# Optimization experiments

Measured on AMD Instinct MI355X. Metric: run time of the kernel, lower is better.

The kernel has to match this reference:

```python
import jax, jax.numpy as jnp
import numpy as np

NUM_CAPSULE = 16
DIM_CAPSULE = 64
ROUTINGS = 3
T_EPS = 1e-7


def setup_inputs() -> dict:
    key = jax.random.key(0)
    k1, k2 = jax.random.split(key)
    x = jax.random.normal(k1, (64, 512, 768), dtype=jnp.float32)
    # xavier-normal-ish init for W: [1, input_dim_capsule, num_capsule*dim_capsule]
    fan_in, fan_out = 768, NUM_CAPSULE * DIM_CAPSULE
    std = float(np.sqrt(2.0 / (fan_in + fan_out)))
    W = jax.random.normal(k2, (1, 768, NUM_CAPSULE * DIM_CAPSULE), dtype=jnp.float32) * std
    return {"x": x, "W": W}


def _squash(v, eps=T_EPS):
    # NOTE: this module's 'squash' is pure L2 normalization with eps, not the
    # classic (s^2/(1+s^2)) squash.
    s2 = jnp.sum(v * v, axis=-1, keepdims=True)
    return v / jnp.sqrt(s2 + eps)


def reference(x, W):
    B, In, _ = x.shape
    # u_hat: [B, In, num*dim] -> [B, num, In, dim]
    u = jnp.matmul(x, W).reshape(B, In, NUM_CAPSULE, DIM_CAPSULE).transpose(0, 2, 1, 3)
    b = jnp.zeros((B, NUM_CAPSULE, In), dtype=u.dtype)  # routing logits
    outputs = None
    for i in range(ROUTINGS):
        # torch code softmaxes over the num_capsule axis (after permute dance)
        c = jax.nn.softmax(b, axis=1)  # [B, num, In]
        outputs = _squash(jnp.einsum('bij,bijk->bik', c, u))  # [B, num, dim]
        if i < ROUTINGS - 1:
            b = jnp.einsum('bik,bijk->bij', outputs, u)  # [B, num, In]
    return outputs
```

## Files before the change

### kernel.cpp

```cpp
#include <hip/hip_runtime.h>
#include <hip/hip_bf16.h>
#include <stdint.h>

#define BATCH 64
#define IN_CAPS 512
#define NCAP 16
#define DCAP 64
#define GN (NCAP * DCAP)
#define GM (BATCH * IN_CAPS)
#define GK 768

typedef __bf16 bf16;
typedef __attribute__((ext_vector_type(8))) __bf16 bf16x8;
typedef __attribute__((ext_vector_type(4))) __bf16 bf16x4;
typedef __attribute__((ext_vector_type(4))) float f32x4;

__global__ void k_detect(const uint32_t* __restrict__ X32, int* __restrict__ flag) {
    const int lane = threadIdx.x;
    int cnt = 0;
#pragma unroll
    for (int i = 0; i < 4; ++i) {
        const uint32_t w = X32[lane * 4 + i];
        const uint32_t e = (w >> 7) & 0xFF;
        cnt += (e >= 119 && e <= 130) ? 1 : 0;
    }
#pragma unroll
    for (int off = 32; off >= 1; off >>= 1) cnt += __shfl_xor(cnt, off);
    if (lane == 0) *flag = (cnt > 128) ? 1 : 0;
}

template <typename T>
__global__ void k_transW(const T* __restrict__ W, bf16* __restrict__ Wt,
                         const int* __restrict__ flag, int want) {
    if (*flag != want) return;
    __shared__ bf16 t[32][33];
    const int k0 = blockIdx.x * 32;
    const int n0 = blockIdx.y * 32;
    const int tx = threadIdx.x, ty = threadIdx.y;
#pragma unroll
    for (int r = 0; r < 4; ++r)
        t[ty + r * 8][tx] = (bf16)(float)W[(size_t)(k0 + ty + r * 8) * GN + n0 + tx];
    __syncthreads();
#pragma unroll
    for (int r = 0; r < 4; ++r)
        Wt[(size_t)(n0 + ty + r * 8) * GK + k0 + tx] = t[tx][ty + r * 8];
}

__device__ inline bf16x8 load8(const bf16* p) { return *(const bf16x8*)p; }
__device__ inline bf16x8 load8(const float* p) {
    const f32x4 a = *(const f32x4*)p;
    const f32x4 b = *(const f32x4*)(p + 4);
    bf16x8 r;
    r[0] = (bf16)a[0]; r[1] = (bf16)a[1]; r[2] = (bf16)a[2]; r[3] = (bf16)a[3];
    r[4] = (bf16)b[0]; r[5] = (bf16)b[1]; r[6] = (bf16)b[2]; r[7] = (bf16)b[3];
    return r;
}

template <typename T>
__global__ __launch_bounds__(256) void k_gemm(const T* __restrict__ X,
                                              const bf16* __restrict__ Wt,
                                              bf16* __restrict__ U,
                                              const int* __restrict__ flag, int want) {
    if (*flag != want) return;
    __shared__ bf16 sA[128 * 32];
    __shared__ bf16 sB[128 * 32];

    const int tid = threadIdx.x;
    const int lane = tid & 63;
    const int wave = tid >> 6;
    const int wm = wave >> 1, wn = wave & 1;
    const int m0 = blockIdx.x * 128;
    const int n0 = blockIdx.y * 128;

    const int srow = tid >> 2;
    const int scol = (tid & 3) * 8;

    f32x4 acc[4][4] = {};

    const int fr = lane & 15;
    const int fq = lane >> 4;

    for (int kt = 0; kt < GK / 32; ++kt) {
        const int kb = kt * 32;
        const bf16x8 a0 = load8(X + (size_t)(m0 + srow) * GK + kb + scol);
        const bf16x8 a1 = load8(X + (size_t)(m0 + srow + 64) * GK + kb + scol);
        const bf16x8 b0 = load8(Wt + (size_t)(n0 + srow) * GK + kb + scol);
        const bf16x8 b1 = load8(Wt + (size_t)(n0 + srow + 64) * GK + kb + scol);

        __syncthreads();
        *(bf16x8*)(sA + srow * 32 + scol) = a0;
        *(bf16x8*)(sA + (srow + 64) * 32 + scol) = a1;
        *(bf16x8*)(sB + srow * 32 + scol) = b0;
        *(bf16x8*)(sB + (srow + 64) * 32 + scol) = b1;
        __syncthreads();

        bf16x8 af[4], bfr[4];
#pragma unroll
        for (int mi = 0; mi < 4; ++mi)
            af[mi] = *(const bf16x8*)(sA + (wm * 64 + mi * 16 + fr) * 32 + fq * 8);
#pragma unroll
        for (int ni = 0; ni < 4; ++ni)
            bfr[ni] = *(const bf16x8*)(sB + (wn * 64 + ni * 16 + fr) * 32 + fq * 8);
#pragma unroll
        for (int mi = 0; mi < 4; ++mi)
#pragma unroll
            for (int ni = 0; ni < 4; ++ni)
                acc[mi][ni] = __builtin_amdgcn_mfma_f32_16x16x32_bf16(
                    af[mi], bfr[ni], acc[mi][ni], 0, 0, 0);
    }

#pragma unroll
    for (int mi = 0; mi < 4; ++mi) {
#pragma unroll
        for (int ni = 0; ni < 4; ++ni) {
#pragma unroll
            for (int r = 0; r < 4; ++r) {
                const int m = m0 + wm * 64 + mi * 16 + fq * 4 + r;
                const int n = n0 + wn * 64 + ni * 16 + fr;
                const int bb = m >> 9, j = m & 511;
                const int ci = n >> 6, k = n & 63;
                U[(((size_t)(bb * NCAP + ci)) * IN_CAPS + j) * DCAP + k] =
                    (bf16)acc[mi][ni][r];
            }
        }
    }
}

__global__ __launch_bounds__(256) void k_caps_out(const bf16* __restrict__ U,
                                                  const float* __restrict__ C,
                                                  float* __restrict__ OutF,
                                                  float* __restrict__ OutC,
                                                  int useC) {
    const int bi = blockIdx.x;
    const int tid = threadIdx.x;
    const int lane = tid & 63, wave = tid >> 6;
    const int kq = lane & 15, jj = lane >> 4;
    const size_t ubase = (size_t)bi * IN_CAPS * DCAP;

    float a0 = 0.f, a1 = 0.f, a2 = 0.f, a3 = 0.f;
#pragma unroll 4
    for (int it = 0; it < 32; ++it) {
        const int j = it * 16 + wave * 4 + jj;
        const bf16x4 v = *(const bf16x4*)(U + ubase + (size_t)j * DCAP + kq * 4);
        const float cv = useC ? C[(size_t)bi * IN_CAPS + j] : 0.0625f;
        a0 += cv * (float)v[0];
        a1 += cv * (float)v[1];
        a2 += cv * (float)v[2];
        a3 += cv * (float)v[3];
    }

    __shared__ float red[16][64];
    const int p = wave * 4 + jj;
    red[p][kq * 4 + 0] = a0;
    red[p][kq * 4 + 1] = a1;
    red[p][kq * 4 + 2] = a2;
    red[p][kq * 4 + 3] = a3;
    __syncthreads();

    if (wave == 0) {
        float s = 0.f;
#pragma unroll
        for (int q = 0; q < 16; ++q) s += red[q][lane];
        float ss = s * s;
#pragma unroll
        for (int off = 32; off >= 1; off >>= 1) ss += __shfl_xor(ss, off);
        const float val = s * rsqrtf(ss + 1e-7f);
        OutF[(size_t)bi * DCAP + lane] = val;
        OutC[(size_t)bi * DCAP + lane] = val;
    }
}

__global__ __launch_bounds__(256) void k_caps_logits(const bf16* __restrict__ U,
                                                     const float* __restrict__ OutF,
                                                     float* __restrict__ BL) {
    const int bi = blockIdx.x;
    const int tid = threadIdx.x;
    const int lane = tid & 63, wave = tid >> 6;
    const int kq = lane & 15, jj = lane >> 4;
    const size_t ubase = (size_t)bi * IN_CAPS * DCAP;

    const float4 ov = *(const float4*)(OutF + (size_t)bi * DCAP + kq * 4);
#pragma unroll 4
    for (int it = 0; it < 32; ++it) {
        const int j = it * 16 + wave * 4 + jj;
        const bf16x4 v = *(const bf16x4*)(U + ubase + (size_t)j * DCAP + kq * 4);
        float p = ov.x * (float)v[0] + ov.y * (float)v[1] +
                  ov.z * (float)v[2] + ov.w * (float)v[3];
        p += __shfl_xor(p, 1);
        p += __shfl_xor(p, 2);
        p += __shfl_xor(p, 4);
        p += __shfl_xor(p, 8);
        if (kq == 0) BL[(size_t)bi * IN_CAPS + j] = p;
    }
}

__global__ __launch_bounds__(256) void k_softmax(float* __restrict__ BL) {
    const int t = blockIdx.x * 256 + threadIdx.x;
    const int b = t >> 9, j = t & 511;
    float* p = BL + (size_t)b * NCAP * IN_CAPS + j;
    float v[16];
    float m = -1e30f;
#pragma unroll
    for (int i = 0; i < 16; ++i) {
        v[i] = p[(size_t)i * IN_CAPS];
        m = fmaxf(m, v[i]);
    }
    float s = 0.f;
#pragma unroll
    for (int i = 0; i < 16; ++i) {
        v[i] = __expf(v[i] - m);
        s += v[i];
    }
    const float inv = 1.0f / s;
#pragma unroll
    for (int i = 0; i < 16; ++i) p[(size_t)i * IN_CAPS] = v[i] * inv;
}

extern "C" void kernel_launch(void* const* d_in, const int* in_sizes, int n_in,
                              void* d_out, int out_size, void* d_ws, size_t ws_size,
                              hipStream_t stream) {
    float* OutC = (float*)d_out;

    const size_t u_bytes = (size_t)BATCH * NCAP * IN_CAPS * DCAP * sizeof(bf16);
    const size_t wt_bytes = (size_t)GN * GK * sizeof(bf16);
    const size_t outf_bytes = (size_t)BATCH * NCAP * DCAP * sizeof(float);
    const size_t bl_bytes = (size_t)BATCH * NCAP * IN_CAPS * sizeof(float);
    char* ws = (char*)d_ws;
    bf16* U = (bf16*)ws;
    bf16* Wt = (bf16*)(ws + u_bytes);
    float* OutF = (float*)(ws + u_bytes + wt_bytes);
    float* BL = (float*)(ws + u_bytes + wt_bytes + outf_bytes);
    int* flag = (int*)(ws + u_bytes + wt_bytes + outf_bytes + bl_bytes);
    if (ws_size < u_bytes + wt_bytes + outf_bytes + bl_bytes + 256) return;

    k_detect<<<1, 64, 0, stream>>>((const uint32_t*)d_in[0], flag);

    k_transW<bf16><<<dim3(GK / 32, GN / 32), dim3(32, 8), 0, stream>>>(
        (const bf16*)d_in[1], Wt, flag, 1);
    k_transW<float><<<dim3(GK / 32, GN / 32), dim3(32, 8), 0, stream>>>(
        (const float*)d_in[1], Wt, flag, 0);

    k_gemm<bf16><<<dim3(GM / 128, GN / 128), 256, 0, stream>>>(
        (const bf16*)d_in[0], Wt, U, flag, 1);
    k_gemm<float><<<dim3(GM / 128, GN / 128), 256, 0, stream>>>(
        (const float*)d_in[0], Wt, U, flag, 0);

    k_caps_out<<<BATCH * NCAP, 256, 0, stream>>>(U, BL, OutF, OutC, 0);
    k_caps_logits<<<BATCH * NCAP, 256, 0, stream>>>(U, OutF, BL);
    k_softmax<<<BATCH * IN_CAPS / 256, 256, 0, stream>>>(BL);
    k_caps_out<<<BATCH * NCAP, 256, 0, stream>>>(U, BL, OutF, OutC, 1);
    k_caps_logits<<<BATCH * NCAP, 256, 0, stream>>>(U, OutF, BL);
    k_softmax<<<BATCH * IN_CAPS / 256, 256, 0, stream>>>(BL);
    k_caps_out<<<BATCH * NCAP, 256, 0, stream>>>(U, BL, OutF, OutC, 1);
}
```

Measured before the change: 298.0 us.

## Pre-convert X to bf16, use async global-to-LDS GEMM loads, fuse routing kernels

Adds a separate pass that converts X to bf16 in workspace, so the GEMM can use direct global-to-LDS loads (global_load_lds) instead of register staging. It also fuses the caps_out and caps_logits kernels into one routing kernel that caches each capsule's 64KB U slice in LDS, so U is read once per iteration instead of twice. The costs are an extra full read and write of X for the conversion, more workspace, and heavy LDS use that limits occupancy in the routing kernel. A fallback keeps the old inline GEMM path when workspace is small.

```diff
diff --git a/kernel.cpp b/kernel.cpp
--- a/kernel.cpp
+++ b/kernel.cpp
@@ -15,6 +15,12 @@
 typedef __attribute__((ext_vector_type(4))) __bf16 bf16x4;
 typedef __attribute__((ext_vector_type(4))) float f32x4;
 
+__device__ inline void async16(const bf16* g, bf16* l) {
+    __builtin_amdgcn_global_load_lds(
+        (__attribute__((address_space(1))) void*)g,
+        (__attribute__((address_space(3))) void*)l, 16, 0, 0);
+}
+
 __global__ void k_detect(const uint32_t* __restrict__ X32, int* __restrict__ flag) {
     const int lane = threadIdx.x;
     int cnt = 0;
@@ -27,6 +33,25 @@
 #pragma unroll
     for (int off = 32; off >= 1; off >>= 1) cnt += __shfl_xor(cnt, off);
     if (lane == 0) *flag = (cnt > 128) ? 1 : 0;
+}
+
+__device__ inline bf16x8 load8(const bf16* p) { return *(const bf16x8*)p; }
+__device__ inline bf16x8 load8(const float* p) {
+    const f32x4 a = *(const f32x4*)p;
+    const f32x4 b = *(const f32x4*)(p + 4);
+    bf16x8 r;
+    r[0] = (bf16)a[0]; r[1] = (bf16)a[1]; r[2] = (bf16)a[2]; r[3] = (bf16)a[3];
+    r[4] = (bf16)b[0]; r[5] = (bf16)b[1]; r[6] = (bf16)b[2]; r[7] = (bf16)b[3];
+    return r;
+}
+
+template <typename T>
+__global__ __launch_bounds__(256) void k_convX(const T* __restrict__ X,
+                                               bf16* __restrict__ Xb,
+                                               const int* __restrict__ flag, int want) {
+    if (*flag != want) return;
+    const size_t i = ((size_t)blockIdx.x * 256 + threadIdx.x) * 8;
+    *(bf16x8*)(Xb + i) = load8(X + i);
 }
 
 template <typename T>
@@ -46,22 +71,9 @@
         Wt[(size_t)(n0 + ty + r * 8) * GK + k0 + tx] = t[tx][ty + r * 8];
 }
 
-__device__ inline bf16x8 load8(const bf16* p) { return *(const bf16x8*)p; }
-__device__ inline bf16x8 load8(const float* p) {
-    const f32x4 a = *(const f32x4*)p;
-    const f32x4 b = *(const f32x4*)(p + 4);
-    bf16x8 r;
-    r[0] = (bf16)a[0]; r[1] = (bf16)a[1]; r[2] = (bf16)a[2]; r[3] = (bf16)a[3];
-    r[4] = (bf16)b[0]; r[5] = (bf16)b[1]; r[6] = (bf16)b[2]; r[7] = (bf16)b[3];
-    return r;
-}
-
-template <typename T>
-__global__ __launch_bounds__(256) void k_gemm(const T* __restrict__ X,
-                                              const bf16* __restrict__ Wt,
-                                              bf16* __restrict__ U,
-                                              const int* __restrict__ flag, int want) {
-    if (*flag != want) return;
+__global__ __launch_bounds__(256) void k_gemm_async(const bf16* __restrict__ Xb,
+                                                    const bf16* __restrict__ Wt,
+                                                    bf16* __restrict__ U) {
     __shared__ bf16 sA[128 * 32];
     __shared__ bf16 sB[128 * 32];
 
@@ -72,26 +84,28 @@
     const int m0 = blockIdx.x * 128;
     const int n0 = blockIdx.y * 128;
 
-    const int srow = tid >> 2;
-    const int scol = (tid & 3) * 8;
+    const int c0 = wave * 2, c1 = wave * 2 + 1;
+    const int rl = lane >> 2, cl = (lane & 3) * 8;
+    const bf16* gA0 = Xb + (size_t)(m0 + c0 * 16 + rl) * GK + cl;
+    const bf16* gA1 = Xb + (size_t)(m0 + c1 * 16 + rl) * GK + cl;
+    const bf16* gB0 = Wt + (size_t)(n0 + c0 * 16 + rl) * GK + cl;
+    const bf16* gB1 = Wt + (size_t)(n0 + c1 * 16 + rl) * GK + cl;
+    bf16* lA0 = sA + c0 * 512;
+    bf16* lA1 = sA + c1 * 512;
+    bf16* lB0 = sB + c0 * 512;
+    bf16* lB1 = sB + c1 * 512;
 
     f32x4 acc[4][4] = {};
-
     const int fr = lane & 15;
     const int fq = lane >> 4;
 
     for (int kt = 0; kt < GK / 32; ++kt) {
-        const int kb = kt * 32;
-        const bf16x8 a0 = load8(X + (size_t)(m0 + srow) * GK + kb + scol);
-        const bf16x8 a1 = load8(X + (size_t)(m0 + srow + 64) * GK + kb + scol);
-        const bf16x8 b0 = load8(Wt + (size_t)(n0 + srow) * GK + kb + scol);
-        const bf16x8 b1 = load8(Wt + (size_t)(n0 + srow + 64) * GK + kb + scol);
-
         __syncthreads();
-        *(bf16x8*)(sA + srow * 32 + scol) = a0;
-        *(bf16x8*)(sA + (srow + 64) * 32 + scol) = a1;
-        *(bf16x8*)(sB + srow * 32 + scol) = b0;
-        *(bf16x8*)(sB + (srow + 64) * 32 + scol) = b1;
+        async16(gA0, lA0);
+        async16(gA1, lA1);
+        async16(gB0, lB0);
+        async16(gB1, lB1);
+        gA0 += 32; gA1 += 32; gB0 += 32; gB1 += 32;
         __syncthreads();
 
         bf16x8 af[4], bfr[4];
@@ -126,30 +140,110 @@
     }
 }
 
-__global__ __launch_bounds__(256) void k_caps_out(const bf16* __restrict__ U,
-                                                  const float* __restrict__ C,
-                                                  float* __restrict__ OutF,
-                                                  float* __restrict__ OutC,
-                                                  int useC) {
+template <typename T>
+__global__ __launch_bounds__(256) void k_gemm_inline(const T* __restrict__ X,
+                                                     const bf16* __restrict__ Wt,
+                                                     bf16* __restrict__ U,
+                                                     const int* __restrict__ flag,
+                                                     int want) {
+    if (*flag != want) return;
+    __shared__ bf16 sA[128 * 32];
+    __shared__ bf16 sB[128 * 32];
+    const int tid = threadIdx.x;
+    const int lane = tid & 63;
+    const int wave = tid >> 6;
+    const int wm = wave >> 1, wn = wave & 1;
+    const int m0 = blockIdx.x * 128;
+    const int n0 = blockIdx.y * 128;
+    const int srow = tid >> 2;
+    const int scol = (tid & 3) * 8;
+    f32x4 acc[4][4] = {};
+    const int fr = lane & 15;
+    const int fq = lane >> 4;
+    for (int kt = 0; kt < GK / 32; ++kt) {
+        const int kb = kt * 32;
+        const bf16x8 a0 = load8(X + (size_t)(m0 + srow) * GK + kb + scol);
+        const bf16x8 a1 = load8(X + (size_t)(m0 + srow + 64) * GK + kb + scol);
+        const bf16x8 b0 = load8(Wt + (size_t)(n0 + srow) * GK + kb + scol);
+        const bf16x8 b1 = load8(Wt + (size_t)(n0 + srow + 64) * GK + kb + scol);
+        __syncthreads();
+        *(bf16x8*)(sA + srow * 32 + scol) = a0;
+        *(bf16x8*)(sA + (srow + 64) * 32 + scol) = a1;
+        *(bf16x8*)(sB + srow * 32 + scol) = b0;
+        *(bf16x8*)(sB + (srow + 64) * 32 + scol) = b1;
+        __syncthreads();
+        bf16x8 af[4], bfr[4];
+#pragma unroll
+        for (int mi = 0; mi < 4; ++mi)
+            af[mi] = *(const bf16x8*)(sA + (wm * 64 + mi * 16 + fr) * 32 + fq * 8);
+#pragma unroll
+        for (int ni = 0; ni < 4; ++ni)
+            bfr[ni] = *(const bf16x8*)(sB + (wn * 64 + ni * 16 + fr) * 32 + fq * 8);
+#pragma unroll
+        for (int mi = 0; mi < 4; ++mi)
+#pragma unroll
+            for (int ni = 0; ni < 4; ++ni)
+                acc[mi][ni] = __builtin_amdgcn_mfma_f32_16x16x32_bf16(
+                    af[mi], bfr[ni], acc[mi][ni], 0, 0, 0);
+    }
+#pragma unroll
+    for (int mi = 0; mi < 4; ++mi) {
+#pragma unroll
+        for (int ni = 0; ni < 4; ++ni) {
+#pragma unroll
+            for (int r = 0; r < 4; ++r) {
+                const int m = m0 + wm * 64 + mi * 16 + fq * 4 + r;
+                const int n = n0 + wn * 64 + ni * 16 + fr;
+                const int bb = m >> 9, j = m & 511;
+                const int ci = n >> 6, k = n & 63;
+                U[(((size_t)(bb * NCAP + ci)) * IN_CAPS + j) * DCAP + k] =
+                    (bf16)acc[mi][ni][r];
+            }
+        }
+    }
+}
+
+__global__ __launch_bounds__(256) void k_route(const bf16* __restrict__ U,
+                                               float* __restrict__ BL,
+                                               float* __restrict__ OutC,
+                                               int mode) {
+    __shared__ bf16 su[IN_CAPS * DCAP];
+    __shared__ float sc[IN_CAPS];
+    __shared__ float red[16][64];
+    __shared__ float sout[64];
     const int bi = blockIdx.x;
     const int tid = threadIdx.x;
+    const size_t ubase = (size_t)bi * IN_CAPS * DCAP;
+
+    {
+        const uint4* g = (const uint4*)(U + ubase);
+        uint4* s = (uint4*)su;
+#pragma unroll
+        for (int i = 0; i < 16; ++i) s[tid + i * 256] = g[tid + i * 256];
+    }
+    if (mode == 0) {
+        sc[tid] = 0.0625f;
+        sc[tid + 256] = 0.0625f;
+    } else {
+        sc[tid] = BL[(size_t)bi * IN_CAPS + tid];
+        sc[tid + 256] = BL[(size_t)bi * IN_CAPS + tid + 256];
+    }
+    __syncthreads();
+
     const int lane = tid & 63, wave = tid >> 6;
     const int kq = lane & 15, jj = lane >> 4;
-    const size_t ubase = (size_t)bi * IN_CAPS * DCAP;
 
     float a0 = 0.f, a1 = 0.f, a2 = 0.f, a3 = 0.f;
-#pragma unroll 4
+#pragma unroll
     for (int it = 0; it < 32; ++it) {
         const int j = it * 16 + wave * 4 + jj;
-        const bf16x4 v = *(const bf16x4*)(U + ubase + (size_t)j * DCAP + kq * 4);
-        const float cv = useC ? C[(size_t)bi * IN_CAPS + j] : 0.0625f;
+        const bf16x4 v = *(const bf16x4*)(su + j * DCAP + kq * 4);
+        const float cv = sc[j];
         a0 += cv * (float)v[0];
         a1 += cv * (float)v[1];
         a2 += cv * (float)v[2];
         a3 += cv * (float)v[3];
     }
-
-    __shared__ float red[16][64];
     const int p = wave * 4 + jj;
     red[p][kq * 4 + 0] = a0;
     red[p][kq * 4 + 1] = a1;
@@ -165,32 +259,24 @@
 #pragma unroll
         for (int off = 32; off >= 1; off >>= 1) ss += __shfl_xor(ss, off);
         const float val = s * rsqrtf(ss + 1e-7f);
-        OutF[(size_t)bi * DCAP + lane] = val;
-        OutC[(size_t)bi * DCAP + lane] = val;
-    }
-}
-
-__global__ __launch_bounds__(256) void k_caps_logits(const bf16* __restrict__ U,
-                                                     const float* __restrict__ OutF,
-                                                     float* __restrict__ BL) {
-    const int bi = blockIdx.x;
-    const int tid = threadIdx.x;
-    const int lane = tid & 63, wave = tid >> 6;
-    const int kq = lane & 15, jj = lane >> 4;
-    const size_t ubase = (size_t)bi * IN_CAPS * DCAP;
-
-    const float4 ov = *(const float4*)(OutF + (size_t)bi * DCAP + kq * 4);
-#pragma unroll 4
+        if (mode == 2) OutC[(size_t)bi * DCAP + lane] = val;
+        sout[lane] = val;
+    }
+    if (mode == 2) return;
+    __syncthreads();
+
+    const float4 ov = *(const float4*)(sout + kq * 4);
+#pragma unroll
     for (int it = 0; it < 32; ++it) {
         const int j = it * 16 + wave * 4 + jj;
-        const bf16x4 v = *(const bf16x4*)(U + ubase + (size_t)j * DCAP + kq * 4);
-        float p = ov.x * (float)v[0] + ov.y * (float)v[1] +
+        const bf16x4 v = *(const bf16x4*)(su + j * DCAP + kq * 4);
+        float q = ov.x * (float)v[0] + ov.y * (float)v[1] +
                   ov.z * (float)v[2] + ov.w * (float)v[3];
-        p += __shfl_xor(p, 1);
-        p += __shfl_xor(p, 2);
-        p += __shfl_xor(p, 4);
-        p += __shfl_xor(p, 8);
-        if (kq == 0) BL[(size_t)bi * IN_CAPS + j] = p;
+        q += __shfl_xor(q, 1);
+        q += __shfl_xor(q, 2);
+        q += __shfl_xor(q, 4);
+        q += __shfl_xor(q, 8);
+        if (kq == 0) BL[(size_t)bi * IN_CAPS + j] = q;
     }
 }
 
@@ -222,34 +308,56 @@
     float* OutC = (float*)d_out;
 
     const size_t u_bytes = (size_t)BATCH * NCAP * IN_CAPS * DCAP * sizeof(bf16);
+    const size_t xb_bytes = (size_t)GM * GK * sizeof(bf16);
     const size_t wt_bytes = (size_t)GN * GK * sizeof(bf16);
-    const size_t outf_bytes = (size_t)BATCH * NCAP * DCAP * sizeof(float);
     const size_t bl_bytes = (size_t)BATCH * NCAP * IN_CAPS * sizeof(float);
     char* ws = (char*)d_ws;
+
+    const size_t need_big = u_bytes + xb_bytes + wt_bytes + bl_bytes + 256;
+    const size_t need_small = u_bytes + wt_bytes + bl_bytes + 256;
+
     bf16* U = (bf16*)ws;
-    bf16* Wt = (bf16*)(ws + u_bytes);
-    float* OutF = (float*)(ws + u_bytes + wt_bytes);
-    float* BL = (float*)(ws + u_bytes + wt_bytes + outf_bytes);
-    int* flag = (int*)(ws + u_bytes + wt_bytes + outf_bytes + bl_bytes);
-    if (ws_size < u_bytes + wt_bytes + outf_bytes + bl_bytes + 256) return;
-
-    k_detect<<<1, 64, 0, stream>>>((const uint32_t*)d_in[0], flag);
-
-    k_transW<bf16><<<dim3(GK / 32, GN / 32), dim3(32, 8), 0, stream>>>(
-        (const bf16*)d_in[1], Wt, flag, 1);
-    k_transW<float><<<dim3(GK / 32, GN / 32), dim3(32, 8), 0, stream>>>(
-        (const float*)d_in[1], Wt, flag, 0);
-
-    k_gemm<bf16><<<dim3(GM / 128, GN / 128), 256, 0, stream>>>(
-        (const bf16*)d_in[0], Wt, U, flag, 1);
-    k_gemm<float><<<dim3(GM / 128, GN / 128), 256, 0, stream>>>(
-        (const float*)d_in[0], Wt, U, flag, 0);
-
-    k_caps_out<<<BATCH * NCAP, 256, 0, stream>>>(U, BL, OutF, OutC, 0);
-    k_caps_logits<<<BATCH * NCAP, 256, 0, stream>>>(U, OutF, BL);
+    bf16* Wt;
+    float* BL;
+    int* flag;
+
+    if (ws_size >= need_big) {
+        bf16* Xb = (bf16*)(ws + u_bytes);
+        Wt = (bf16*)(ws + u_bytes + xb_bytes);
+        BL = (float*)(ws + u_bytes + xb_bytes + wt_bytes);
+        flag = (int*)(ws + u_bytes + xb_bytes + wt_bytes + bl_bytes);
+
+        k_detect<<<1, 64, 0, stream>>>((const uint32_t*)d_in[0], flag);
+        k_convX<bf16><<<GM * GK / (256 * 8), 256, 0, stream>>>(
+            (const bf16*)d_in[0], Xb, flag, 1);
+        k_convX<float><<<GM * GK / (256 * 8), 256, 0, stream>>>(
+            (const float*)d_in[0], Xb, flag, 0);
+        k_transW<bf16><<<dim3(GK / 32, GN / 32), dim3(32, 8), 0, stream>>>(
+            (const bf16*)d_in[1], Wt, flag, 1);
+        k_transW<float><<<dim3(GK / 32, GN / 32), dim3(32, 8), 0, stream>>>(
+            (const float*)d_in[1], Wt, flag, 0);
+        k_gemm_async<<<dim3(GM / 128, GN / 128), 256, 0, stream>>>(Xb, Wt, U);
+    } else if (ws_size >= need_small) {
+        Wt = (bf16*)(ws + u_bytes);
+        BL = (float*)(ws + u_bytes + wt_bytes);
+        flag = (int*)(ws + u_bytes + wt_bytes + bl_bytes);
+
+        k_detect<<<1, 64, 0, stream>>>((const uint32_t*)d_in[0], flag);
+        k_transW<bf16><<<dim3(GK / 32, GN / 32), dim3(32, 8), 0, stream>>>(
+            (const bf16*)d_in[1], Wt, flag, 1);
+        k_transW<float><<<dim3(GK / 32, GN / 32), dim3(32, 8), 0, stream>>>(
+            (const float*)d_in[1], Wt, flag, 0);
+        k_gemm_inline<bf16><<<dim3(GM / 128, GN / 128), 256, 0, stream>>>(
+            (const bf16*)d_in[0], Wt, U, flag, 1);
+        k_gemm_inline<float><<<dim3(GM / 128, GN / 128), 256, 0, stream>>>(
+            (const float*)d_in[0], Wt, U, flag, 0);
+    } else {
+        return;
+    }
+
+    k_route<<<BATCH * NCAP, 256, 0, stream>>>(U, BL, OutC, 0);
     k_softmax<<<BATCH * IN_CAPS / 256, 256, 0, stream>>>(BL);
-    k_caps_out<<<BATCH * NCAP, 256, 0, stream>>>(U, BL, OutF, OutC, 1);
-    k_caps_logits<<<BATCH * NCAP, 256, 0, stream>>>(U, OutF, BL);
+    k_route<<<BATCH * NCAP, 256, 0, stream>>>(U, BL, OutC, 1);
     k_softmax<<<BATCH * IN_CAPS / 256, 256, 0, stream>>>(BL);
-    k_caps_out<<<BATCH * NCAP, 256, 0, stream>>>(U, BL, OutF, OutC, 1);
-}
+    k_route<<<BATCH * NCAP, 256, 0, stream>>>(U, BL, OutC, 2);
+}
```

Result: no change. 298.8 us (+0.3%).
